# Performance work log

Measured on AMD Instinct MI355X. Metric: run time of the kernel, lower is better.

The kernel has to match this reference:

```python
import jax, jax.numpy as jnp
import numpy as np

N_HEADS = 16
N_DIM = 1024
H_DIM = N_DIM // N_HEADS


def setup_inputs() -> dict:
    key = jax.random.key(0)
    ks = jax.random.split(key, 9)
    s = 1.0 / np.sqrt(N_DIM)
    x = jax.random.normal(ks[0], (4, 2048, N_DIM), dtype=jnp.float32)
    Wq = jax.random.uniform(ks[1], (N_DIM, N_DIM), jnp.float32, -s, s)
    bq = jax.random.uniform(ks[2], (N_DIM,), jnp.float32, -s, s)
    Wk = jax.random.uniform(ks[3], (N_DIM, N_DIM), jnp.float32, -s, s)
    bk = jax.random.uniform(ks[4], (N_DIM,), jnp.float32, -s, s)
    Wv = jax.random.uniform(ks[5], (N_DIM, N_DIM), jnp.float32, -s, s)
    bv = jax.random.uniform(ks[6], (N_DIM,), jnp.float32, -s, s)
    Wp = jax.random.uniform(ks[7], (N_DIM, N_DIM), jnp.float32, -s, s)
    bp = jax.random.uniform(ks[8], (N_DIM,), jnp.float32, -s, s)
    return {"x": x, "Wq": Wq, "bq": bq, "Wk": Wk, "bk": bk,
            "Wv": Wv, "bv": bv, "Wp": Wp, "bp": bp}


def _split_heads(y):
    # [b, t, (nh*hd)] -> [nh, b, t, hd]
    b, t, _ = y.shape
    return y.reshape(b, t, N_HEADS, H_DIM).transpose(2, 0, 1, 3)


def reference(x, Wq, bq, Wk, bk, Wv, bv, Wp, bp):
    q = _split_heads(x @ Wq.T + bq)
    k = _split_heads(x @ Wk.T + bk)
    v = _split_heads(x @ Wv.T + bv)
    # NOTE: original module applies NO 1/sqrt(d) scaling
    energies = jnp.einsum('hbqd,hbkd->hbqk', q, k)
    attn = jax.nn.softmax(energies, axis=-1)  # dropout disabled (eval)
    out = jnp.einsum('hbqk,hbkd->hbqd', attn, v)
    # [nh, b, t, hd] -> [b, t, nh*hd]
    b, t = out.shape[1], out.shape[2]
    out = out.transpose(1, 2, 0, 3).reshape(b, t, N_DIM)
    return out @ Wp.T + bp
```

## Files before the change

### kernel.cpp

```cpp
#include <hip/hip_runtime.h>
#include <hip/hip_bf16.h>


typedef short short8 __attribute__((ext_vector_type(8)));
typedef float float4v __attribute__((ext_vector_type(4)));

#define MFMA16(a, b, c) __builtin_amdgcn_mfma_f32_16x16x32_bf16((a), (b), (c), 0, 0, 0)
#define LOG2E 1.4426950408889634f

#define B_SZ 4
#define T_SZ 2048
#define D_SZ 1024
#define NH 16
#define HD 64
#define M_SZ (B_SZ * T_SZ)
#define MW_SZ (D_SZ * D_SZ)

__device__ __forceinline__ unsigned short f2bf(float f) {
  unsigned int u = __float_as_uint(f);
  u += 0x7fffu + ((u >> 16) & 1u);
  return (unsigned short)(u >> 16);
}

__device__ __forceinline__ float fexp2(float x) {
#if __has_builtin(__builtin_amdgcn_exp2f)
  return __builtin_amdgcn_exp2f(x);
#else
  return exp2f(x);
#endif
}

__device__ __forceinline__ void gl_lds16(const unsigned short* g, unsigned short* l) {
  __builtin_amdgcn_global_load_lds(
      (const __attribute__((address_space(1))) unsigned int*)g,
      (__attribute__((address_space(3))) unsigned int*)l, 16, 0, 0);
}

__global__ __launch_bounds__(256) void cvt_all(const float* __restrict__ x,
                                               const float* __restrict__ w0,
                                               const float* __restrict__ w1,
                                               const float* __restrict__ w2,
                                               const float* __restrict__ w3,
                                               const float* __restrict__ b0,
                                               const float* __restrict__ b1,
                                               const float* __restrict__ b2,
                                               unsigned short* __restrict__ xb,
                                               unsigned short* __restrict__ wout,
                                               float* __restrict__ bout) {
  const long blk = blockIdx.x;
  if (blk < 8192) {
    long i = (blk * 256 + threadIdx.x) * 4;
    float4 v = *(const float4*)(x + i);
    uint2 o;
    o.x = (unsigned)f2bf(v.x) | ((unsigned)f2bf(v.y) << 16);
    o.y = (unsigned)f2bf(v.z) | ((unsigned)f2bf(v.w) << 16);
    *(uint2*)(xb + i) = o;
  } else if (blk < 12288) {
    long i = ((blk - 8192) * 256 + threadIdx.x) * 4;
    int which = (int)(i >> 20);
    const float* src = which == 0 ? w0 : which == 1 ? w1 : which == 2 ? w2 : w3;
    float scale = which == 0 ? LOG2E : 1.0f;
    long j = i - (long)which * MW_SZ;
    float4 v = *(const float4*)(src + j);
    uint2 o;
    o.x = (unsigned)f2bf(v.x * scale) | ((unsigned)f2bf(v.y * scale) << 16);
    o.y = (unsigned)f2bf(v.z * scale) | ((unsigned)f2bf(v.w * scale) << 16);
    *(uint2*)(wout + i) = o;
  } else {
    int i = (int)((blk - 12288) * 256 + threadIdx.x) * 4;
    float4 v;
    if (i < 1024) {
      v = *(const float4*)(b0 + i);
      v.x *= LOG2E; v.y *= LOG2E; v.z *= LOG2E; v.w *= LOG2E;
    } else if (i < 2048) {
      v = *(const float4*)(b1 + (i - 1024));
    } else {
      v = *(const float4*)(b2 + (i - 2048));
    }
    *(float4*)(bout + i) = v;
  }
}

__global__ __launch_bounds__(256, 3) void gemm_qkv(const unsigned short* __restrict__ A,
                                                   const unsigned short* __restrict__ W,
                                                   const float* __restrict__ bias,
                                                   unsigned short* __restrict__ Qb,
                                                   unsigned short* __restrict__ Kb,
                                                   unsigned short* __restrict__ Vt) {
  __shared__ __align__(16) unsigned short smem[17408];
  unsigned short* As = smem;
  unsigned short* Bs = smem + 8192;
  unsigned short* Ct = smem;
  const int tid = threadIdx.x;
  const int wave = tid >> 6, lane = tid & 63;
  const int q = lane >> 4, ln = lane & 15;
  const int wm = (wave >> 1) * 64, wn = (wave & 1) * 64;
  const int bid = blockIdx.x;
  const int r8 = bid & 7, g = bid >> 3;
  const long m0 = (long)(r8 + 8 * (g & 7)) * 128;
  const long n0 = (long)(g >> 3) * 128;
  const int srow = lane >> 3, scol = (lane & 7) * 8;
  const int K = D_SZ;

  float4v acc[4][4] = {};

  for (int k0 = 0; k0 < K; k0 += 64) {
    for (int t = 0; t < 4; ++t) {
      int seg = wave * 4 + t;
      int row = seg * 8 + srow;
      gl_lds16(A + (m0 + row) * (long)K + k0 + scol, As + seg * 512);
      gl_lds16(W + (n0 + row) * (long)K + k0 + scol, Bs + seg * 512);
    }
    __syncthreads();
    for (int ks = 0; ks < 2; ++ks) {
      short8 af[4], bf[4];
      for (int i = 0; i < 4; ++i)
        af[i] = *(const short8*)(As + (wm + i * 16 + ln) * 64 + ks * 32 + q * 8);
      for (int j = 0; j < 4; ++j)
        bf[j] = *(const short8*)(Bs + (wn + j * 16 + ln) * 64 + ks * 32 + q * 8);
      for (int i = 0; i < 4; ++i)
        for (int j = 0; j < 4; ++j)
          acc[i][j] = MFMA16(af[i], bf[j], acc[i][j]);
    }
    __syncthreads();
  }

  if ((int)n0 < 2048) {
    unsigned short* dst = (int)n0 < 1024 ? Qb : Kb;
    int coff = (int)n0 < 1024 ? 0 : 1024;
    for (int i = 0; i < 4; ++i) {
      long rowb = m0 + wm + i * 16 + q * 4;
      for (int j = 0; j < 4; ++j) {
        long col = n0 + wn + j * 16 + ln;
        float bv = bias[col];
        for (int r = 0; r < 4; ++r)
          dst[(rowb + r) * (long)D_SZ + col - coff] = f2bf(acc[i][j][r] + bv);
      }
    }
  } else {
    for (int i = 0; i < 4; ++i)
      for (int j = 0; j < 4; ++j) {
        int col_l = wn + j * 16 + ln;
        float bv = bias[n0 + col_l];
        __hip_bfloat162 lo =
            __float22bfloat162_rn(make_float2(acc[i][j][0] + bv, acc[i][j][1] + bv));
        __hip_bfloat162 hi =
            __float22bfloat162_rn(make_float2(acc[i][j][2] + bv, acc[i][j][3] + bv));
        uint2 w;
        w.x = *(unsigned*)&lo;
        w.y = *(unsigned*)&hi;
        *(uint2*)(Ct + col_l * 136 + wm + i * 16 + q * 4) = w;
      }
    __syncthreads();
    for (int it = 0; it < 8; ++it) {
      int idx = tid + it * 256;
      int c = idx >> 4, rb = idx & 15;
      uint4 v = *(const uint4*)(Ct + c * 136 + rb * 8);
      *(uint4*)(Vt + (n0 - 2048 + c) * (long)M_SZ + m0 + rb * 8) = v;
    }
  }
}

__global__ __launch_bounds__(256, 3) void gemm_proj(const unsigned short* __restrict__ A,
                                                    const unsigned short* __restrict__ W,
                                                    const float* __restrict__ bias,
                                                    float* __restrict__ Cf) {
  __shared__ __align__(16) unsigned short As[128 * 64];
  __shared__ __align__(16) unsigned short Bs[128 * 64];
  const int tid = threadIdx.x;
  const int wave = tid >> 6, lane = tid & 63;
  const int q = lane >> 4, ln = lane & 15;
  const int wm = (wave >> 1) * 64, wn = (wave & 1) * 64;
  const int bid = blockIdx.x;
  const int r8 = bid & 7, g = bid >> 3;
  const long m0 = (long)(r8 + 8 * (g & 7)) * 128;
  const long n0 = (long)(g >> 3) * 128;
  const int srow = lane >> 3, scol = (lane & 7) * 8;
  const int K = D_SZ;

  float4v acc[4][4] = {};
  for (int k0 = 0; k0 < K; k0 += 64) {
    for (int t = 0; t < 4; ++t) {
      int seg = wave * 4 + t;
      int row = seg * 8 + srow;
      gl_lds16(A + (m0 + row) * (long)K + k0 + scol, As + seg * 512);
      gl_lds16(W + (n0 + row) * (long)K + k0 + scol, Bs + seg * 512);
    }
    __syncthreads();
    for (int ks = 0; ks < 2; ++ks) {
      short8 af[4], bf[4];
      for (int i = 0; i < 4; ++i)
        af[i] = *(const short8*)(As + (wm + i * 16 + ln) * 64 + ks * 32 + q * 8);
      for (int j = 0; j < 4; ++j)
        bf[j] = *(const short8*)(Bs + (wn + j * 16 + ln) * 64 + ks * 32 + q * 8);
      for (int i = 0; i < 4; ++i)
        for (int j = 0; j < 4; ++j)
          acc[i][j] = MFMA16(af[i], bf[j], acc[i][j]);
    }
    __syncthreads();
  }
  for (int i = 0; i < 4; ++i) {
    long rowb = m0 + wm + i * 16 + q * 4;
    for (int j = 0; j < 4; ++j) {
      long col = n0 + wn + j * 16 + ln;
      float bv = bias[col];
      for (int r = 0; r < 4; ++r)
        Cf[(rowb + r) * (long)D_SZ + col] = acc[i][j][r] + bv;
    }
  }
}

__global__ __launch_bounds__(512, 4) void attn_kernel(const unsigned short* __restrict__ Qb,
                                                      const unsigned short* __restrict__ Kb,
                                                      const unsigned short* __restrict__ Vt,
                                                      unsigned short* __restrict__ Ob) {
  __shared__ __align__(16) unsigned short KV[16384];
  __shared__ __align__(16) unsigned short Pp[10240];

  const int tid = threadIdx.x;
  const int wave = tid >> 6, lane = tid & 63;
  const int q = lane >> 4, ln = lane & 15;
  const int l7 = lane & 7, l3 = lane >> 3;
  const int bid = blockIdx.x;
  const int qt = bid >> 6;
  const int hb = bid & 63;
  const int h = hb & 15, b = hb >> 4;

  const long baseQ = ((long)b * T_SZ + qt * 256) * D_SZ + h * HD;
  const long baseK = (long)b * T_SZ * D_SZ + h * HD;
  const long baseV = (long)h * HD * M_SZ + (long)b * T_SZ;
  const int cs = ((l7 ^ l3) * 8);

  short8 qf[2][2];
  for (int i = 0; i < 2; ++i)
    for (int ks = 0; ks < 2; ++ks)
      qf[i][ks] = *(const short8*)(Qb + baseQ + (long)(wave * 32 + i * 16 + ln) * D_SZ +
                                   ks * 32 + q * 8);

  float4v o[2][4] = {};
  float lp[2] = {};
  unsigned short* Ppw = Pp + wave * (32 * 40);
  const int swz = (ln & 7) * 8;

#define STAGE(kt_, base_)                                                                \
  {                                                                                      \
    int row = wave * 8 + l3;                                                             \
    gl_lds16(Kb + baseK + (long)((kt_)*64 + row) * D_SZ + cs, (base_) + wave * 512);     \
    gl_lds16(Vt + baseV + (long)row * M_SZ + (kt_)*64 + cs, (base_) + 4096 + wave * 512);\
  }

  STAGE(0, KV)

  for (int kt = 0; kt < 32; ++kt) {
    unsigned short* cur = KV + (kt & 1) * 8192;
    unsigned short* nxt = KV + ((kt & 1) ^ 1) * 8192;
    __syncthreads();
    if (kt < 31) { STAGE(kt + 1, nxt) }

    short8 kf[4][2];
    for (int c = 0; c < 4; ++c)
      for (int ks = 0; ks < 2; ++ks)
        kf[c][ks] = *(const short8*)(cur + (c * 16 + ln) * 64 + ((ks * 32 + q * 8) ^ swz));
    float4v s[4][2];
    for (int c = 0; c < 4; ++c)
      for (int i = 0; i < 2; ++i) {
        float4v z = {};
        z = MFMA16(kf[c][0], qf[i][0], z);
        z = MFMA16(kf[c][1], qf[i][1], z);
        s[c][i] = z;
      }

    for (int ks = 0; ks < 2; ++ks) {
      for (int i = 0; i < 2; ++i)
        for (int cl = 0; cl < 2; ++cl) {
          int c = 2 * ks + cl;
          float p0 = fexp2(s[c][i][0]);
          float p1 = fexp2(s[c][i][1]);
          float p2 = fexp2(s[c][i][2]);
          float p3 = fexp2(s[c][i][3]);
          lp[i] += (p0 + p1) + (p2 + p3);
          __hip_bfloat162 lo = __float22bfloat162_rn(make_float2(p0, p1));
          __hip_bfloat162 hi = __float22bfloat162_rn(make_float2(p2, p3));
          uint2 w;
          w.x = *(unsigned*)&lo;
          w.y = *(unsigned*)&hi;
          *(uint2*)(Ppw + (i * 16 + ln) * 40 + cl * 16 + q * 4) = w;
        }
      short8 vf[4];
      for (int j = 0; j < 4; ++j)
        vf[j] = *(const short8*)(cur + 4096 + (j * 16 + ln) * 64 + ((ks * 32 + q * 8) ^ swz));
      short8 pf[2];
      for (int i = 0; i < 2; ++i)
        pf[i] = *(const short8*)(Ppw + (i * 16 + ln) * 40 + q * 8);
      for (int i = 0; i < 2; ++i)
        for (int j = 0; j < 4; ++j)
          o[i][j] = MFMA16(pf[i], vf[j], o[i][j]);
    }
  }

  for (int i = 0; i < 2; ++i) {
    float l = lp[i];
    l += __shfl_xor(l, 16, 64);
    l += __shfl_xor(l, 32, 64);
    float inv = 1.f / l;
    for (int r = 0; r < 4; ++r) {
      int src = (lane & 48) | (q * 4 + r);
      float invr = __shfl(inv, src, 64);
      int row = qt * 256 + wave * 32 + i * 16 + q * 4 + r;
      long base = ((long)b * T_SZ + row) * D_SZ + h * HD;
      for (int j = 0; j < 4; ++j)
        Ob[base + j * 16 + ln] = f2bf(o[i][j][r] * invr);
    }
  }
#undef STAGE
}

extern "C" void kernel_launch(void* const* d_in, const int* in_sizes, int n_in,
                              void* d_out, int out_size, void* d_ws, size_t ws_size,
                              hipStream_t stream) {
  const float* x = (const float*)d_in[0];
  const float* Wq = (const float*)d_in[1];
  const float* bq = (const float*)d_in[2];
  const float* Wk = (const float*)d_in[3];
  const float* bk = (const float*)d_in[4];
  const float* Wv = (const float*)d_in[5];
  const float* bv = (const float*)d_in[6];
  const float* Wp = (const float*)d_in[7];
  const float* bp = (const float*)d_in[8];
  float* out = (float*)d_out;

  const long MX = (long)M_SZ * D_SZ;
  const long MW = (long)MW_SZ;
  unsigned short* ws = (unsigned short*)d_ws;
  unsigned short* xb = ws;
  unsigned short* Wcat = xb + MX;
  float* bcat = (float*)(Wcat + 4 * MW);
  unsigned short* Qb = (unsigned short*)(bcat + 3072);
  unsigned short* Kb = Qb + MX;
  unsigned short* Vtb = Kb + MX;
  unsigned short* Ob = Vtb + MX;

  cvt_all<<<12291, 256, 0, stream>>>(x, Wq, Wk, Wv, Wp, bq, bk, bv, xb, Wcat, bcat);

  gemm_qkv<<<1536, 256, 0, stream>>>(xb, Wcat, bcat, Qb, Kb, Vtb);

  attn_kernel<<<512, 512, 0, stream>>>(Qb, Kb, Vtb, Ob);

  gemm_proj<<<512, 256, 0, stream>>>(Ob, Wcat + 3 * MW, bp, out);
}
```

Before: 265.2 us.

## Double-buffer GEMM LDS tiles and XOR-swizzle attention P scratch

Both projection GEMMs now use two LDS stage buffers, prefetching the next K-slice while computing the current one. This removes one barrier per iteration and hides global-load latency, at the cost of doubling LDS to 64KB and lowering launch bounds from 3 to 2 blocks per CU. The attention kernel's per-wave P scratch drops its padded 40-element stride for a 32-element stride with an XOR swizzle, shrinking LDS use while aiming to keep bank conflicts low.

Result: no change. 266.9 us (+0.6%).

```diff
diff --git a/kernel.cpp b/kernel.cpp
--- a/kernel.cpp
+++ b/kernel.cpp
@@ -81,15 +81,13 @@
   }
 }
 
-__global__ __launch_bounds__(256, 3) void gemm_qkv(const unsigned short* __restrict__ A,
+__global__ __launch_bounds__(256, 2) void gemm_qkv(const unsigned short* __restrict__ A,
                                                    const unsigned short* __restrict__ W,
                                                    const float* __restrict__ bias,
                                                    unsigned short* __restrict__ Qb,
                                                    unsigned short* __restrict__ Kb,
                                                    unsigned short* __restrict__ Vt) {
-  __shared__ __align__(16) unsigned short smem[17408];
-  unsigned short* As = smem;
-  unsigned short* Bs = smem + 8192;
+  __shared__ __align__(16) unsigned short smem[32768];
   unsigned short* Ct = smem;
   const int tid = threadIdx.x;
   const int wave = tid >> 6, lane = tid & 63;
@@ -104,14 +102,22 @@
 
   float4v acc[4][4] = {};
 
-  for (int k0 = 0; k0 < K; k0 += 64) {
-    for (int t = 0; t < 4; ++t) {
-      int seg = wave * 4 + t;
-      int row = seg * 8 + srow;
-      gl_lds16(A + (m0 + row) * (long)K + k0 + scol, As + seg * 512);
-      gl_lds16(W + (n0 + row) * (long)K + k0 + scol, Bs + seg * 512);
-    }
-    __syncthreads();
+#define STG(k0_, buf_)                                                              \
+  for (int t_ = 0; t_ < 4; ++t_) {                                                  \
+    int seg = wave * 4 + t_;                                                        \
+    int row = seg * 8 + srow;                                                       \
+    gl_lds16(A + (m0 + row) * (long)K + (k0_) + scol, smem + (buf_)*16384 + seg*512); \
+    gl_lds16(W + (n0 + row) * (long)K + (k0_) + scol,                               \
+             smem + (buf_)*16384 + 8192 + seg * 512);                               \
+  }
+
+  STG(0, 0)
+
+  for (int t = 0; t < 16; ++t) {
+    const unsigned short* As = smem + (t & 1) * 16384;
+    const unsigned short* Bs = As + 8192;
+    __syncthreads();
+    if (t < 15) { STG((t + 1) * 64, (t & 1) ^ 1) }
     for (int ks = 0; ks < 2; ++ks) {
       short8 af[4], bf[4];
       for (int i = 0; i < 4; ++i)
@@ -122,8 +128,8 @@
         for (int j = 0; j < 4; ++j)
           acc[i][j] = MFMA16(af[i], bf[j], acc[i][j]);
     }
-    __syncthreads();
-  }
+  }
+#undef STG
 
   if ((int)n0 < 2048) {
     unsigned short* dst = (int)n0 < 1024 ? Qb : Kb;
@@ -138,6 +144,7 @@
       }
     }
   } else {
+    __syncthreads();
     for (int i = 0; i < 4; ++i)
       for (int j = 0; j < 4; ++j) {
         int col_l = wn + j * 16 + ln;
@@ -161,12 +168,11 @@
   }
 }
 
-__global__ __launch_bounds__(256, 3) void gemm_proj(const unsigned short* __restrict__ A,
+__global__ __launch_bounds__(256, 2) void gemm_proj(const unsigned short* __restrict__ A,
                                                     const unsigned short* __restrict__ W,
                                                     const float* __restrict__ bias,
                                                     float* __restrict__ Cf) {
-  __shared__ __align__(16) unsigned short As[128 * 64];
-  __shared__ __align__(16) unsigned short Bs[128 * 64];
+  __shared__ __align__(16) unsigned short smem[32768];
   const int tid = threadIdx.x;
   const int wave = tid >> 6, lane = tid & 63;
   const int q = lane >> 4, ln = lane & 15;
@@ -179,14 +185,23 @@
   const int K = D_SZ;
 
   float4v acc[4][4] = {};
-  for (int k0 = 0; k0 < K; k0 += 64) {
-    for (int t = 0; t < 4; ++t) {
-      int seg = wave * 4 + t;
-      int row = seg * 8 + srow;
-      gl_lds16(A + (m0 + row) * (long)K + k0 + scol, As + seg * 512);
-      gl_lds16(W + (n0 + row) * (long)K + k0 + scol, Bs + seg * 512);
-    }
-    __syncthreads();
+
+#define STG(k0_, buf_)                                                              \
+  for (int t_ = 0; t_ < 4; ++t_) {                                                  \
+    int seg = wave * 4 + t_;                                                        \
+    int row = seg * 8 + srow;                                                       \
+    gl_lds16(A + (m0 + row) * (long)K + (k0_) + scol, smem + (buf_)*16384 + seg*512); \
+    gl_lds16(W + (n0 + row) * (long)K + (k0_) + scol,                               \
+             smem + (buf_)*16384 + 8192 + seg * 512);                               \
+  }
+
+  STG(0, 0)
+
+  for (int t = 0; t < 16; ++t) {
+    const unsigned short* As = smem + (t & 1) * 16384;
+    const unsigned short* Bs = As + 8192;
+    __syncthreads();
+    if (t < 15) { STG((t + 1) * 64, (t & 1) ^ 1) }
     for (int ks = 0; ks < 2; ++ks) {
       short8 af[4], bf[4];
       for (int i = 0; i < 4; ++i)
@@ -197,8 +212,9 @@
         for (int j = 0; j < 4; ++j)
           acc[i][j] = MFMA16(af[i], bf[j], acc[i][j]);
     }
-    __syncthreads();
-  }
+  }
+#undef STG
+
   for (int i = 0; i < 4; ++i) {
     long rowb = m0 + wm + i * 16 + q * 4;
     for (int j = 0; j < 4; ++j) {
@@ -215,7 +231,7 @@
                                                       const unsigned short* __restrict__ Vt,
                                                       unsigned short* __restrict__ Ob) {
   __shared__ __align__(16) unsigned short KV[16384];
-  __shared__ __align__(16) unsigned short Pp[10240];
+  __shared__ __align__(16) unsigned short Pp[8192];
 
   const int tid = threadIdx.x;
   const int wave = tid >> 6, lane = tid & 63;
@@ -239,7 +255,7 @@
 
   float4v o[2][4] = {};
   float lp[2] = {};
-  unsigned short* Ppw = Pp + wave * (32 * 40);
+  unsigned short* Ppw = Pp + wave * 1024;
   const int swz = (ln & 7) * 8;
 
 #define STAGE(kt_, base_)                                                                \
@@ -284,14 +300,15 @@
           uint2 w;
           w.x = *(unsigned*)&lo;
           w.y = *(unsigned*)&hi;
-          *(uint2*)(Ppw + (i * 16 + ln) * 40 + cl * 16 + q * 4) = w;
+          int o8 = 2 * cl + (q >> 1);
+          *(uint2*)(Ppw + (i * 16 + ln) * 32 + ((o8 ^ (ln & 3)) * 8) + (q & 1) * 4) = w;
         }
       short8 vf[4];
       for (int j = 0; j < 4; ++j)
         vf[j] = *(const short8*)(cur + 4096 + (j * 16 + ln) * 64 + ((ks * 32 + q * 8) ^ swz));
       short8 pf[2];
       for (int i = 0; i < 2; ++i)
-        pf[i] = *(const short8*)(Ppw + (i * 16 + ln) * 40 + q * 8);
+        pf[i] = *(const short8*)(Ppw + (i * 16 + ln) * 32 + ((q ^ (ln & 3)) * 8));
       for (int i = 0; i < 2; ++i)
         for (int j = 0; j < 4; ++j)
           o[i][j] = MFMA16(pf[i], vf[j], o[i][j]);
```
